# Performance work log

Hardware: AMD Instinct MI355X
Metric: run time of the kernel (lower is better)

## Reference

```python
import jax, jax.numpy as jnp
import numpy as np

B, T, D, H = 8, 4096, 512, 512


def log_g(x):
    # log of g(x) where g(x) = relu(x) + 0.5 for x >= 0, sigmoid(x) for x < 0
    return jnp.where(x >= 0, jnp.log(jax.nn.relu(x) + 0.5), -jax.nn.softplus(-x))


def setup_inputs() -> dict:
    key = jax.random.key(0)
    kx, kh0, kwz, kbz, kwh, kbh = jax.random.split(key, 6)
    s = 1.0 / np.sqrt(D)
    return {
        "x": jax.random.normal(kx, (B, T, D), dtype=jnp.float32),
        "h_0": jax.random.uniform(kh0, (B, H), dtype=jnp.float32),
        "Wz": jax.random.uniform(kwz, (H, D), dtype=jnp.float32, minval=-s, maxval=s),
        "bz": jax.random.uniform(kbz, (H,), dtype=jnp.float32, minval=-s, maxval=s),
        "Wh": jax.random.uniform(kwh, (H, D), dtype=jnp.float32, minval=-s, maxval=s),
        "bh": jax.random.uniform(kbh, (H,), dtype=jnp.float32, minval=-s, maxval=s),
    }


def parallel_scan_log(log_coeffs, log_values):
    # log_coeffs: (B, T, H), log_values: (B, T+1, H)
    a_star = jnp.cumsum(jnp.pad(log_coeffs, ((0, 0), (1, 0), (0, 0))), axis=1)  # (B, T+1, H)
    log_h = a_star + jax.lax.cumlogsumexp(log_values - a_star, axis=1)
    return jnp.exp(log_h)  # (B, T+1, H)


def reference(x, h_0, Wz, bz, Wh, bh):
    k = jnp.einsum('btd,hd->bth', x, Wz) + bz                # (B, T, H)
    log_z = -jax.nn.softplus(-k)                              # log sigmoid(k)
    log_coeffs = -jax.nn.softplus(k)                          # log (1 - sigmoid(k))
    log_h0 = log_g(h_0)[:, None, :]                           # (B, 1, H)
    log_tilde_h = log_g(jnp.einsum('btd,hd->bth', x, Wh) + bh)
    vals = jnp.concatenate([log_h0, log_z + log_tilde_h], axis=1)  # (B, T+1, H)
    h = parallel_scan_log(log_coeffs, vals)
    return h[:, -x.shape[1]:, :]                              # (B, T, H)
```

## Files before the change

kernel.cpp:

```cpp
#include <hip/hip_runtime.h>
#include <math.h>

#define Bq 8
#define Tq 4096
#define Dq 512
#define Hq 512
#define Mq (Bq * Tq)
#define NC 64
#define CL 64

typedef unsigned short ushort_t;
typedef unsigned int uint_t;
typedef __bf16 bf16x8 __attribute__((ext_vector_type(8)));
typedef float f32x4 __attribute__((ext_vector_type(4)));

__device__ __forceinline__ ushort_t f2bf(float f) {
    unsigned int u = __float_as_uint(f);
    unsigned int r = u + 0x7fffu + ((u >> 16) & 1u);
    return (ushort_t)(r >> 16);
}

__device__ __forceinline__ void gload16(const void* g, void* l) {
    __builtin_amdgcn_global_load_lds(
        (const __attribute__((address_space(1))) void*)g,
        (__attribute__((address_space(3))) void*)l, 16, 0, 0);
}

__device__ __forceinline__ void gates(uint_t w, float& c, float& v) {
    float k  = __uint_as_float((w & 0xffffu) << 16);
    float th = __uint_as_float(w & 0xffff0000u);
    float ek = __expf(k);
    c = 1.0f / (1.0f + ek);
    float z = 1.0f - c;
    float g = (th >= 0.0f) ? (th + 0.5f) : (1.0f / (1.0f + __expf(-th)));
    v = z * g;
}

__global__ __launch_bounds__(256)
void convert_all(const float* __restrict__ x, const float* __restrict__ Wz,
                 const float* __restrict__ Wh, ushort_t* __restrict__ dst) {
    size_t i8 = ((size_t)blockIdx.x * 256 + threadIdx.x) * 8;
    const size_t XN = (size_t)Mq * Dq;
    const size_t WN = (size_t)Hq * Dq;
    const float* src; size_t off;
    if (i8 < XN)            { src = x;  off = i8; }
    else if (i8 < XN + WN)  { src = Wz; off = i8 - XN; }
    else                    { src = Wh; off = i8 - XN - WN; }
    float4 a = *reinterpret_cast<const float4*>(src + off);
    float4 b = *reinterpret_cast<const float4*>(src + off + 4);
    uint4 o;
    o.x = (uint_t)f2bf(a.x) | ((uint_t)f2bf(a.y) << 16);
    o.y = (uint_t)f2bf(a.z) | ((uint_t)f2bf(a.w) << 16);
    o.z = (uint_t)f2bf(b.x) | ((uint_t)f2bf(b.y) << 16);
    o.w = (uint_t)f2bf(b.z) | ((uint_t)f2bf(b.w) << 16);
    *reinterpret_cast<uint4*>(dst + i8) = o;
}

__global__ __launch_bounds__(256, 2)
void gemm_fused(const ushort_t* __restrict__ xb, const ushort_t* __restrict__ wb,
                const float* __restrict__ bz, const float* __restrict__ bh,
                uint_t* __restrict__ kvout) {
    __shared__ __align__(16) ushort_t As [128 * 64];
    __shared__ __align__(16) ushort_t Bzs[128 * 64];
    __shared__ __align__(16) ushort_t Bhs[128 * 64];

    const int tid  = threadIdx.x;
    const int lane = tid & 63;
    const int wave = tid >> 6;
    const int wm = (wave >> 1) * 64;
    const int wn = (wave & 1) * 64;
    const int mBase = blockIdx.x * 128;
    const int nBase = blockIdx.y * 128;
    const ushort_t* Wzb = wb;
    const ushort_t* Whb = wb + (size_t)Hq * Dq;

    f32x4 zero = {0.f, 0.f, 0.f, 0.f};
    f32x4 accz[4][4], acch[4][4];
#pragma unroll
    for (int i = 0; i < 4; ++i)
#pragma unroll
        for (int j = 0; j < 4; ++j) { accz[i][j] = zero; acch[i][j] = zero; }

    const int rowInW = lane >> 3;
    const int ccG = (lane & 7) ^ rowInW;
    const int swz = lane & 7;

    for (int k0 = 0; k0 < Dq; k0 += 64) {
#pragma unroll
        for (int j = 0; j < 4; ++j) {
            const int rseg = j * 4 + wave;
            const int row  = rseg * 8 + rowInW;
            const size_t gcol = (size_t)(k0 + ccG * 8);
            gload16(xb  + (size_t)(mBase + row) * Dq + gcol, &As [rseg * 512]);
            gload16(Wzb + (size_t)(nBase + row) * Dq + gcol, &Bzs[rseg * 512]);
            gload16(Whb + (size_t)(nBase + row) * Dq + gcol, &Bhs[rseg * 512]);
        }
        __syncthreads();

#pragma unroll
        for (int ks = 0; ks < 2; ++ks) {
            const int cc = ks * 4 + (lane >> 4);
            const int sc = cc ^ swz;
            bf16x8 af[4], bzf[4], bhf[4];
#pragma unroll
            for (int i = 0; i < 4; ++i) {
                int rowA = wm + i * 16 + (lane & 15);
                af[i] = *reinterpret_cast<const bf16x8*>(&As[rowA * 64 + sc * 8]);
            }
#pragma unroll
            for (int i = 0; i < 4; ++i) {
                int rowB = wn + i * 16 + (lane & 15);
                bzf[i] = *reinterpret_cast<const bf16x8*>(&Bzs[rowB * 64 + sc * 8]);
                bhf[i] = *reinterpret_cast<const bf16x8*>(&Bhs[rowB * 64 + sc * 8]);
            }
#pragma unroll
            for (int mi = 0; mi < 4; ++mi)
#pragma unroll
                for (int ni = 0; ni < 4; ++ni) {
                    accz[mi][ni] = __builtin_amdgcn_mfma_f32_16x16x32_bf16(
                        af[mi], bzf[ni], accz[mi][ni], 0, 0, 0);
                    acch[mi][ni] = __builtin_amdgcn_mfma_f32_16x16x32_bf16(
                        af[mi], bhf[ni], acch[mi][ni], 0, 0, 0);
                }
        }
        __syncthreads();
    }

    const int colL = lane & 15;
    const int rowQ = (lane >> 4) * 4;
#pragma unroll
    for (int mi = 0; mi < 4; ++mi) {
#pragma unroll
        for (int ni = 0; ni < 4; ++ni) {
            int h = nBase + wn + ni * 16 + colL;
            float bzv = bz[h];
            float bhv = bh[h];
#pragma unroll
            for (int r = 0; r < 4; ++r) {
                int bt = mBase + wm + mi * 16 + rowQ + r;
                float kf  = accz[mi][ni][r] + bzv;
                float thf = acch[mi][ni][r] + bhv;
                kvout[(size_t)bt * Hq + h] =
                    (uint_t)f2bf(kf) | ((uint_t)f2bf(thf) << 16);
            }
        }
    }
}

__global__ __launch_bounds__(256)
void scan_partials(const uint_t* __restrict__ kv, float4* __restrict__ chAW) {
    const int b = blockIdx.x >> 6;
    const int chunk = blockIdx.x & 63;
    const int h2 = threadIdx.x;
    const uint2* kv2 = reinterpret_cast<const uint2*>(kv);
    size_t base = ((size_t)b * Tq + (size_t)chunk * CL) * (Hq / 2) + h2;
    float A0 = 1.f, W0 = 0.f, A1 = 1.f, W1 = 0.f;
#pragma unroll 8
    for (int t = 0; t < CL; ++t) {
        uint2 w = kv2[base + (size_t)t * (Hq / 2)];
        float c0, v0, c1, v1;
        gates(w.x, c0, v0);
        gates(w.y, c1, v1);
        W0 = fmaf(c0, W0, v0); A0 *= c0;
        W1 = fmaf(c1, W1, v1); A1 *= c1;
    }
    chAW[(size_t)blockIdx.x * (Hq / 2) + h2] = make_float4(A0, W0, A1, W1);
}

__global__ __launch_bounds__(256)
void scan_combine(const float* __restrict__ h0, const float4* __restrict__ chAW,
                  float2* __restrict__ hstart) {
    int idx = blockIdx.x * 256 + threadIdx.x;
    float2 x0 = reinterpret_cast<const float2*>(h0)[idx];
    int b = idx >> 8;
    int h2 = idx & 255;
    float r0 = (x0.x >= 0.f) ? (x0.x + 0.5f) : (1.f / (1.f + __expf(-x0.x)));
    float r1 = (x0.y >= 0.f) ? (x0.y + 0.5f) : (1.f / (1.f + __expf(-x0.y)));
    for (int c = 0; c < NC; ++c) {
        size_t o = ((size_t)b * NC + c) * (Hq / 2) + h2;
        hstart[o] = make_float2(r0, r1);
        float4 aw = chAW[o];
        r0 = fmaf(aw.x, r0, aw.y);
        r1 = fmaf(aw.z, r1, aw.w);
    }
}

__global__ __launch_bounds__(256)
void scan_final(const uint_t* kv, const float2* __restrict__ hstart, float* out) {
    const int b = blockIdx.x >> 6;
    const int chunk = blockIdx.x & 63;
    const int h2 = threadIdx.x;
    float2 hs = hstart[(size_t)blockIdx.x * (Hq / 2) + h2];
    float r0 = hs.x, r1 = hs.y;
    const uint2* kv2 = reinterpret_cast<const uint2*>(kv);
    float2* out2 = reinterpret_cast<float2*>(out);
    size_t base = ((size_t)b * Tq + (size_t)chunk * CL) * (Hq / 2) + h2;

    uint2 w[8];
#pragma unroll
    for (int j = 0; j < 8; ++j) w[j] = kv2[base + (size_t)j * (Hq / 2)];

    for (int bt = 0; bt < 8; ++bt) {
        uint2 wn[8];
        if (bt < 7) {
#pragma unroll
            for (int j = 0; j < 8; ++j)
                wn[j] = kv2[base + (size_t)((bt + 1) * 8 + j) * (Hq / 2)];
        }
#pragma unroll
        for (int j = 0; j < 8; ++j) {
            float c0, v0, c1, v1;
            gates(w[j].x, c0, v0);
            gates(w[j].y, c1, v1);
            r0 = fmaf(c0, r0, v0);
            r1 = fmaf(c1, r1, v1);
            out2[base + (size_t)(bt * 8 + j) * (Hq / 2)] = make_float2(r0, r1);
        }
#pragma unroll
        for (int j = 0; j < 8; ++j) w[j] = wn[j];
    }
}

extern "C" void kernel_launch(void* const* d_in, const int* in_sizes, int n_in,
                              void* d_out, int out_size, void* d_ws, size_t ws_size,
                              hipStream_t stream) {
    const float* x  = (const float*)d_in[0];
    const float* h0 = (const float*)d_in[1];
    const float* Wz = (const float*)d_in[2];
    const float* bz = (const float*)d_in[3];
    const float* Wh = (const float*)d_in[4];
    const float* bh = (const float*)d_in[5];
    float* out = (float*)d_out;

    char* ws = (char*)d_ws;
    ushort_t* xb = (ushort_t*)ws;
    ushort_t* wb = xb + (size_t)Mq * Dq;
    float4* chAW = (float4*)(wb + 2 * (size_t)Hq * Dq);
    float2* hstart = (float2*)((char*)chAW + (size_t)Bq * NC * (Hq / 2) * 16);
    uint_t* kv = (uint_t*)d_out;

    const int totalConv = (Mq * Dq + 2 * Hq * Dq) / (256 * 8);
    convert_all<<<dim3(totalConv), dim3(256), 0, stream>>>(x, Wz, Wh, xb);
    gemm_fused<<<dim3(Mq / 128, Hq / 128), dim3(256), 0, stream>>>(xb, wb, bz, bh, kv);
    scan_partials<<<dim3(Bq * NC), dim3(256), 0, stream>>>(kv, chAW);
    scan_combine<<<dim3(Bq), dim3(256), 0, stream>>>(h0, chAW, hstart);
    scan_final<<<dim3(Bq * NC), dim3(256), 0, stream>>>(kv, hstart, out);
}
```

Before: 218.6 us.

## Fuse chunk scan partials into GEMM epilogue and parallelize combine over H

Computes per-chunk (A, W) scan partials directly in the GEMM epilogue from the freshly computed bf16 gate words, combining per-lane partials through shared memory, and removes the separate scan_partials kernel that re-read the whole kv buffer. The combine kernel is relaid to one thread per hidden unit with 16 blocks and batched prefetch of chunk partials. This removes a full pass over kv and a launch, at the cost of extra gate math and shared-memory traffic in the GEMM epilogue. Chunk length stays 64 rows, matching scan_final.

Measured after the change: 199.7 us. 1.09x faster.

```diff
diff --git a/kernel.cpp b/kernel.cpp
--- a/kernel.cpp
+++ b/kernel.cpp
@@ -59,10 +59,11 @@
 __global__ __launch_bounds__(256, 2)
 void gemm_fused(const ushort_t* __restrict__ xb, const ushort_t* __restrict__ wb,
                 const float* __restrict__ bz, const float* __restrict__ bh,
-                uint_t* __restrict__ kvout) {
-    __shared__ __align__(16) ushort_t As [128 * 64];
-    __shared__ __align__(16) ushort_t Bzs[128 * 64];
-    __shared__ __align__(16) ushort_t Bhs[128 * 64];
+                uint_t* __restrict__ kvout, float2* __restrict__ chAW) {
+    __shared__ __align__(16) ushort_t smem[3 * 128 * 64];
+    ushort_t* As  = smem;
+    ushort_t* Bzs = smem + 128 * 64;
+    ushort_t* Bhs = smem + 2 * 128 * 64;
 
     const int tid  = threadIdx.x;
     const int lane = tid & 63;
@@ -127,70 +128,74 @@
     }
 
     const int colL = lane & 15;
-    const int rowQ = (lane >> 4) * 4;
-#pragma unroll
-    for (int mi = 0; mi < 4; ++mi) {
-#pragma unroll
-        for (int ni = 0; ni < 4; ++ni) {
-            int h = nBase + wn + ni * 16 + colL;
-            float bzv = bz[h];
-            float bhv = bh[h];
+    const int quad = lane >> 4;
+    float2* sb = reinterpret_cast<float2*>(smem) + wave * 1024;
+
+#pragma unroll
+    for (int ni = 0; ni < 4; ++ni) {
+        int h = nBase + wn + ni * 16 + colL;
+        float bzv = bz[h];
+        float bhv = bh[h];
+#pragma unroll
+        for (int mi = 0; mi < 4; ++mi) {
+            float A = 1.f, W = 0.f;
 #pragma unroll
             for (int r = 0; r < 4; ++r) {
-                int bt = mBase + wm + mi * 16 + rowQ + r;
+                int bt = mBase + wm + mi * 16 + quad * 4 + r;
                 float kf  = accz[mi][ni][r] + bzv;
                 float thf = acch[mi][ni][r] + bhv;
-                kvout[(size_t)bt * Hq + h] =
-                    (uint_t)f2bf(kf) | ((uint_t)f2bf(thf) << 16);
+                uint_t word = (uint_t)f2bf(kf) | ((uint_t)f2bf(thf) << 16);
+                kvout[(size_t)bt * Hq + h] = word;
+                float c, v;
+                gates(word, c, v);
+                W = fmaf(c, W, v);
+                A *= c;
             }
-        }
+            sb[(mi * 4 + quad) * 64 + ni * 16 + colL] = make_float2(A, W);
+        }
+    }
+    __syncthreads();
+    {
+        float A = 1.f, W = 0.f;
+#pragma unroll
+        for (int s = 0; s < 16; ++s) {
+            float2 aw = sb[s * 64 + lane];
+            W = fmaf(aw.x, W, aw.y);
+            A *= aw.x;
+        }
+        int g = blockIdx.x * 2 + (wm >> 6);
+        int h = nBase + wn + lane;
+        chAW[(size_t)g * Hq + h] = make_float2(A, W);
     }
 }
 
 __global__ __launch_bounds__(256)
-void scan_partials(const uint_t* __restrict__ kv, float4* __restrict__ chAW) {
+void scan_combine(const float* __restrict__ h0, const float2* __restrict__ chAW,
+                  float* __restrict__ hstart) {
+    int idx = blockIdx.x * 256 + threadIdx.x;
+    int b = idx >> 9;
+    int h = idx & (Hq - 1);
+    float x0 = h0[idx];
+    float r = (x0 >= 0.f) ? (x0 + 0.5f) : (1.f / (1.f + __expf(-x0)));
+    const float2* p = chAW + (size_t)b * NC * Hq + h;
+    for (int c0 = 0; c0 < NC; c0 += 16) {
+        float2 aw[16];
+#pragma unroll
+        for (int j = 0; j < 16; ++j) aw[j] = p[(size_t)(c0 + j) * Hq];
+#pragma unroll
+        for (int j = 0; j < 16; ++j) {
+            hstart[((size_t)b * NC + c0 + j) * Hq + h] = r;
+            r = fmaf(aw[j].x, r, aw[j].y);
+        }
+    }
+}
+
+__global__ __launch_bounds__(256)
+void scan_final(const uint_t* kv, const float* __restrict__ hstart, float* out) {
     const int b = blockIdx.x >> 6;
     const int chunk = blockIdx.x & 63;
     const int h2 = threadIdx.x;
-    const uint2* kv2 = reinterpret_cast<const uint2*>(kv);
-    size_t base = ((size_t)b * Tq + (size_t)chunk * CL) * (Hq / 2) + h2;
-    float A0 = 1.f, W0 = 0.f, A1 = 1.f, W1 = 0.f;
-#pragma unroll 8
-    for (int t = 0; t < CL; ++t) {
-        uint2 w = kv2[base + (size_t)t * (Hq / 2)];
-        float c0, v0, c1, v1;
-        gates(w.x, c0, v0);
-        gates(w.y, c1, v1);
-        W0 = fmaf(c0, W0, v0); A0 *= c0;
-        W1 = fmaf(c1, W1, v1); A1 *= c1;
-    }
-    chAW[(size_t)blockIdx.x * (Hq / 2) + h2] = make_float4(A0, W0, A1, W1);
-}
-
-__global__ __launch_bounds__(256)
-void scan_combine(const float* __restrict__ h0, const float4* __restrict__ chAW,
-                  float2* __restrict__ hstart) {
-    int idx = blockIdx.x * 256 + threadIdx.x;
-    float2 x0 = reinterpret_cast<const float2*>(h0)[idx];
-    int b = idx >> 8;
-    int h2 = idx & 255;
-    float r0 = (x0.x >= 0.f) ? (x0.x + 0.5f) : (1.f / (1.f + __expf(-x0.x)));
-    float r1 = (x0.y >= 0.f) ? (x0.y + 0.5f) : (1.f / (1.f + __expf(-x0.y)));
-    for (int c = 0; c < NC; ++c) {
-        size_t o = ((size_t)b * NC + c) * (Hq / 2) + h2;
-        hstart[o] = make_float2(r0, r1);
-        float4 aw = chAW[o];
-        r0 = fmaf(aw.x, r0, aw.y);
-        r1 = fmaf(aw.z, r1, aw.w);
-    }
-}
-
-__global__ __launch_bounds__(256)
-void scan_final(const uint_t* kv, const float2* __restrict__ hstart, float* out) {
-    const int b = blockIdx.x >> 6;
-    const int chunk = blockIdx.x & 63;
-    const int h2 = threadIdx.x;
-    float2 hs = hstart[(size_t)blockIdx.x * (Hq / 2) + h2];
+    float2 hs = reinterpret_cast<const float2*>(hstart)[(size_t)blockIdx.x * (Hq / 2) + h2];
     float r0 = hs.x, r1 = hs.y;
     const uint2* kv2 = reinterpret_cast<const uint2*>(kv);
     float2* out2 = reinterpret_cast<float2*>(out);
@@ -235,14 +240,13 @@
     char* ws = (char*)d_ws;
     ushort_t* xb = (ushort_t*)ws;
     ushort_t* wb = xb + (size_t)Mq * Dq;
-    float4* chAW = (float4*)(wb + 2 * (size_t)Hq * Dq);
-    float2* hstart = (float2*)((char*)chAW + (size_t)Bq * NC * (Hq / 2) * 16);
+    float2* chAW = (float2*)(wb + 2 * (size_t)Hq * Dq);
+    float* hstart = (float*)((char*)chAW + (size_t)Bq * NC * Hq * sizeof(float2));
     uint_t* kv = (uint_t*)d_out;
 
     const int totalConv = (Mq * Dq + 2 * Hq * Dq) / (256 * 8);
     convert_all<<<dim3(totalConv), dim3(256), 0, stream>>>(x, Wz, Wh, xb);
-    gemm_fused<<<dim3(Mq / 128, Hq / 128), dim3(256), 0, stream>>>(xb, wb, bz, bh, kv);
-    scan_partials<<<dim3(Bq * NC), dim3(256), 0, stream>>>(kv, chAW);
-    scan_combine<<<dim3(Bq), dim3(256), 0, stream>>>(h0, chAW, hstart);
+    gemm_fused<<<dim3(Mq / 128, Hq / 128), dim3(256), 0, stream>>>(xb, wb, bz, bh, kv, chAW);
+    scan_combine<<<dim3((Bq * Hq) / 256), dim3(256), 0, stream>>>(h0, chAW, hstart);
     scan_final<<<dim3(Bq * NC), dim3(256), 0, stream>>>(kv, hstart, out);
 }
```

## Fuse three scan kernels into one pass with device-wide atomic counters

Applied to the files above, without the earlier changes.

Replaces the scan_partials, scan_combine and scan_final launches with a single kernel. Blocks publish chunk partials and bump a per-batch atomic counter; chunk 0 waits on it, combines the partials into start states and raises a flag that the other blocks spin on. This removes two kernel launches and the boundaries between them, and also batches the partial-pass loads 16 at a time. The risk is that waiting blocks may deadlock if they occupy the GPU before chunk 0 runs; here 512 blocks of 256 threads are expected to all be resident on MI355X.

After: 479.2 us. 2.19x slower.

```diff
diff --git a/kernel.cpp b/kernel.cpp
--- a/kernel.cpp
+++ b/kernel.cpp
@@ -5,6 +5,7 @@
 #define Tq 4096
 #define Dq 512
 #define Hq 512
+#define H2 (Hq / 2)
 #define Mq (Bq * Tq)
 #define NC 64
 #define CL 64
@@ -38,7 +39,9 @@
 
 __global__ __launch_bounds__(256)
 void convert_all(const float* __restrict__ x, const float* __restrict__ Wz,
-                 const float* __restrict__ Wh, ushort_t* __restrict__ dst) {
+                 const float* __restrict__ Wh, ushort_t* __restrict__ dst,
+                 uint_t* __restrict__ sync) {
+    if (blockIdx.x == 0 && threadIdx.x < 16) sync[threadIdx.x] = 0;
     size_t i8 = ((size_t)blockIdx.x * 256 + threadIdx.x) * 8;
     const size_t XN = (size_t)Mq * Dq;
     const size_t WN = (size_t)Hq * Dq;
@@ -147,65 +150,76 @@
     }
 }
 
-__global__ __launch_bounds__(256)
-void scan_partials(const uint_t* __restrict__ kv, float4* __restrict__ chAW) {
-    const int b = blockIdx.x >> 6;
-    const int chunk = blockIdx.x & 63;
+__global__ __launch_bounds__(256, 4)
+void scan_onepass(const float* __restrict__ h0, float4* chAW, float2* hstart,
+                  uint_t* cnt, uint_t* flag, float* out) {
+    const int blk = blockIdx.x;
+    const int b = blk >> 6;
+    const int c = blk & 63;
     const int h2 = threadIdx.x;
-    const uint2* kv2 = reinterpret_cast<const uint2*>(kv);
-    size_t base = ((size_t)b * Tq + (size_t)chunk * CL) * (Hq / 2) + h2;
+    const uint2* kv2 = reinterpret_cast<const uint2*>(out);
+    float2* out2 = reinterpret_cast<float2*>(out);
+    const size_t base = ((size_t)b * Tq + (size_t)c * CL) * H2 + h2;
+
     float A0 = 1.f, W0 = 0.f, A1 = 1.f, W1 = 0.f;
-#pragma unroll 8
-    for (int t = 0; t < CL; ++t) {
-        uint2 w = kv2[base + (size_t)t * (Hq / 2)];
-        float c0, v0, c1, v1;
-        gates(w.x, c0, v0);
-        gates(w.y, c1, v1);
-        W0 = fmaf(c0, W0, v0); A0 *= c0;
-        W1 = fmaf(c1, W1, v1); A1 *= c1;
-    }
-    chAW[(size_t)blockIdx.x * (Hq / 2) + h2] = make_float4(A0, W0, A1, W1);
-}
-
-__global__ __launch_bounds__(256)
-void scan_combine(const float* __restrict__ h0, const float4* __restrict__ chAW,
-                  float2* __restrict__ hstart) {
-    int idx = blockIdx.x * 256 + threadIdx.x;
-    float2 x0 = reinterpret_cast<const float2*>(h0)[idx];
-    int b = idx >> 8;
-    int h2 = idx & 255;
-    float r0 = (x0.x >= 0.f) ? (x0.x + 0.5f) : (1.f / (1.f + __expf(-x0.x)));
-    float r1 = (x0.y >= 0.f) ? (x0.y + 0.5f) : (1.f / (1.f + __expf(-x0.y)));
-    for (int c = 0; c < NC; ++c) {
-        size_t o = ((size_t)b * NC + c) * (Hq / 2) + h2;
-        hstart[o] = make_float2(r0, r1);
-        float4 aw = chAW[o];
-        r0 = fmaf(aw.x, r0, aw.y);
-        r1 = fmaf(aw.z, r1, aw.w);
-    }
-}
-
-__global__ __launch_bounds__(256)
-void scan_final(const uint_t* kv, const float2* __restrict__ hstart, float* out) {
-    const int b = blockIdx.x >> 6;
-    const int chunk = blockIdx.x & 63;
-    const int h2 = threadIdx.x;
-    float2 hs = hstart[(size_t)blockIdx.x * (Hq / 2) + h2];
+    for (int t0 = 0; t0 < CL; t0 += 16) {
+        uint2 w[16];
+#pragma unroll
+        for (int j = 0; j < 16; ++j) w[j] = kv2[base + (size_t)(t0 + j) * H2];
+#pragma unroll
+        for (int j = 0; j < 16; ++j) {
+            float c0, v0, c1, v1;
+            gates(w[j].x, c0, v0);
+            gates(w[j].y, c1, v1);
+            W0 = fmaf(c0, W0, v0); A0 *= c0;
+            W1 = fmaf(c1, W1, v1); A1 *= c1;
+        }
+    }
+    chAW[(size_t)blk * H2 + h2] = make_float4(A0, W0, A1, W1);
+    __threadfence();
+    __syncthreads();
+    if (threadIdx.x == 0)
+        __hip_atomic_fetch_add(&cnt[b], 1u, __ATOMIC_RELEASE, __HIP_MEMORY_SCOPE_AGENT);
+
+    if (c == 0) {
+        while (__hip_atomic_load(&cnt[b], __ATOMIC_ACQUIRE, __HIP_MEMORY_SCOPE_AGENT) < NC)
+            __builtin_amdgcn_s_sleep(16);
+        float2 x0 = reinterpret_cast<const float2*>(h0)[b * H2 + h2];
+        float r0 = (x0.x >= 0.f) ? (x0.x + 0.5f) : (1.f / (1.f + __expf(-x0.x)));
+        float r1 = (x0.y >= 0.f) ? (x0.y + 0.5f) : (1.f / (1.f + __expf(-x0.y)));
+        const float4* p = chAW + (size_t)b * NC * H2 + h2;
+        float2* q = hstart + (size_t)b * NC * H2 + h2;
+        for (int c0 = 0; c0 < NC; c0 += 8) {
+            float4 aw[8];
+#pragma unroll
+            for (int j = 0; j < 8; ++j) aw[j] = p[(size_t)(c0 + j) * H2];
+#pragma unroll
+            for (int j = 0; j < 8; ++j) {
+                q[(size_t)(c0 + j) * H2] = make_float2(r0, r1);
+                r0 = fmaf(aw[j].x, r0, aw[j].y);
+                r1 = fmaf(aw[j].z, r1, aw[j].w);
+            }
+        }
+        __threadfence();
+        __syncthreads();
+        if (threadIdx.x == 0)
+            __hip_atomic_store(&flag[b], 1u, __ATOMIC_RELEASE, __HIP_MEMORY_SCOPE_AGENT);
+    }
+
+    while (__hip_atomic_load(&flag[b], __ATOMIC_ACQUIRE, __HIP_MEMORY_SCOPE_AGENT) == 0)
+        __builtin_amdgcn_s_sleep(16);
+
+    float2 hs = hstart[(size_t)blk * H2 + h2];
     float r0 = hs.x, r1 = hs.y;
-    const uint2* kv2 = reinterpret_cast<const uint2*>(kv);
-    float2* out2 = reinterpret_cast<float2*>(out);
-    size_t base = ((size_t)b * Tq + (size_t)chunk * CL) * (Hq / 2) + h2;
-
     uint2 w[8];
 #pragma unroll
-    for (int j = 0; j < 8; ++j) w[j] = kv2[base + (size_t)j * (Hq / 2)];
-
+    for (int j = 0; j < 8; ++j) w[j] = kv2[base + (size_t)j * H2];
     for (int bt = 0; bt < 8; ++bt) {
         uint2 wn[8];
         if (bt < 7) {
 #pragma unroll
             for (int j = 0; j < 8; ++j)
-                wn[j] = kv2[base + (size_t)((bt + 1) * 8 + j) * (Hq / 2)];
+                wn[j] = kv2[base + (size_t)((bt + 1) * 8 + j) * H2];
         }
 #pragma unroll
         for (int j = 0; j < 8; ++j) {
@@ -214,7 +228,7 @@
             gates(w[j].y, c1, v1);
             r0 = fmaf(c0, r0, v0);
             r1 = fmaf(c1, r1, v1);
-            out2[base + (size_t)(bt * 8 + j) * (Hq / 2)] = make_float2(r0, r1);
+            out2[base + (size_t)(bt * 8 + j) * H2] = make_float2(r0, r1);
         }
 #pragma unroll
         for (int j = 0; j < 8; ++j) w[j] = wn[j];
@@ -236,13 +250,14 @@
     ushort_t* xb = (ushort_t*)ws;
     ushort_t* wb = xb + (size_t)Mq * Dq;
     float4* chAW = (float4*)(wb + 2 * (size_t)Hq * Dq);
-    float2* hstart = (float2*)((char*)chAW + (size_t)Bq * NC * (Hq / 2) * 16);
+    float2* hstart = (float2*)((char*)chAW + (size_t)Bq * NC * H2 * sizeof(float4));
+    uint_t* sync = (uint_t*)((char*)hstart + (size_t)Bq * NC * H2 * sizeof(float2));
+    uint_t* cnt = sync;
+    uint_t* flag = sync + 8;
     uint_t* kv = (uint_t*)d_out;
 
     const int totalConv = (Mq * Dq + 2 * Hq * Dq) / (256 * 8);
-    convert_all<<<dim3(totalConv), dim3(256), 0, stream>>>(x, Wz, Wh, xb);
+    convert_all<<<dim3(totalConv), dim3(256), 0, stream>>>(x, Wz, Wh, xb, sync);
     gemm_fused<<<dim3(Mq / 128, Hq / 128), dim3(256), 0, stream>>>(xb, wb, bz, bh, kv);
-    scan_partials<<<dim3(Bq * NC), dim3(256), 0, stream>>>(kv, chAW);
-    scan_combine<<<dim3(Bq), dim3(256), 0, stream>>>(h0, chAW, hstart);
-    scan_final<<<dim3(Bq * NC), dim3(256), 0, stream>>>(kv, hstart, out);
-}
+    scan_onepass<<<dim3(Bq * NC), dim3(256), 0, stream>>>(h0, chAW, hstart, cnt, flag, out);
+}
```
